# Performance work log

Measured on AMD Instinct MI355X. Metric: run time of the kernel, lower is better.

## Reference

```python
import jax, jax.numpy as jnp
import numpy as np

B, L, D, H = 4, 1024, 1024, 16
HD = D // H  # 64
MAX_LEN = 1024


def setup_inputs() -> dict:
    key = jax.random.key(0)
    k1, k2, k3, k4 = jax.random.split(key, 4)
    x = jax.random.normal(k1, (B, L, D), dtype=jnp.float32)
    W_qkv = jax.random.normal(k2, (D, 3 * D), dtype=jnp.float32) * (1.0 / np.sqrt(D))
    W_proj = jax.random.normal(k3, (D, D), dtype=jnp.float32) * (1.0 / np.sqrt(D))
    b_proj = jnp.zeros((D,), dtype=jnp.float32)
    rel_pos_emb = jax.random.normal(k4, (2 * MAX_LEN - 1, HD), dtype=jnp.float32)
    return {"x": x, "W_qkv": W_qkv, "W_proj": W_proj, "b_proj": b_proj,
            "rel_pos_emb": rel_pos_emb}


def reference(x, W_qkv, W_proj, b_proj, rel_pos_emb):
    b, l, d = x.shape
    scale = 1.0 / np.sqrt(HD)
    # fused qkv projection: [B, L, 3, H, HD]
    qkv = (x @ W_qkv).reshape(b, l, 3, H, HD)
    q = jnp.transpose(qkv[:, :, 0], (0, 2, 1, 3))  # [B, H, L, HD]
    k = jnp.transpose(qkv[:, :, 1], (0, 2, 1, 3))
    v = jnp.transpose(qkv[:, :, 2], (0, 2, 1, 3))
    # content scores
    attn = jnp.einsum('bhld,bhmd->bhlm', q, k) * scale
    # relative position scores: pos_indices[i, j] = (j - i) + (L - 1)
    pos_indices = (jnp.arange(l)[None, :] - jnp.arange(l)[:, None]) + (l - 1)
    rel_pos = rel_pos_emb[pos_indices]  # [L, L, HD]
    pos_attn = jnp.einsum('bhld,lkd->bhlk', q, rel_pos) * scale
    attn = jax.nn.softmax(attn + pos_attn, axis=-1)
    out = jnp.einsum('bhlm,bhmd->bhld', attn, v)  # [B, H, L, HD]
    out = jnp.transpose(out, (0, 2, 1, 3)).reshape(b, l, d)
    return out @ W_proj + b_proj
```

## Files before the change

kernel.cpp:

```cpp
#include <hip/hip_runtime.h>
#include <cstdint>

#define L_SEQ 1024
#define NH 16
#define HD 64
#define DMODEL 1024
#define BHS (L_SEQ * HD)

typedef __bf16 bf16x8 __attribute__((ext_vector_type(8)));
typedef float f32x4 __attribute__((ext_vector_type(4)));
typedef unsigned short u16x8 __attribute__((ext_vector_type(8)));

#define MFMA16(a, b, c) __builtin_amdgcn_mfma_f32_16x16x32_bf16((a), (b), (c), 0, 0, 0)

static __device__ __forceinline__ unsigned short f2b(float f) {
  unsigned int u = __builtin_bit_cast(unsigned int, f);
  u = (u + 0x7FFFu + ((u >> 16) & 1u)) >> 16;
  return (unsigned short)u;
}

static __device__ __forceinline__ bf16x8 ld8(const unsigned short* p) {
  return *(const bf16x8*)(p);
}

static __device__ __forceinline__ float bperm(int byteaddr, float v) {
  return __builtin_bit_cast(float,
      __builtin_amdgcn_ds_bpermute(byteaddr, __builtin_bit_cast(int, v)));
}

static __device__ __forceinline__ void gl_lds(const unsigned short* g,
                                              unsigned short* l) {
  auto gp = (const __attribute__((address_space(1))) unsigned int*)((uintptr_t)g);
  auto lp = (__attribute__((address_space(3))) unsigned int*)((uintptr_t)l);
  __builtin_amdgcn_global_load_lds(gp, lp, 16, 0, 0);
}

__global__ __launch_bounds__(256) void k_prep(
    const float* __restrict__ x,      unsigned short* __restrict__ xb,
    const float* __restrict__ relemb, unsigned short* __restrict__ eb,
    const float* __restrict__ Wqkv,   unsigned short* __restrict__ wtq,
    const float* __restrict__ Wproj,  unsigned short* __restrict__ wtp) {
  const int b = blockIdx.x, tid = threadIdx.x;
  if (b < 4224) {
    const float* src; unsigned short* dst; int i;
    if (b < 4096) { src = x; dst = xb; i = b * 256 + tid; }
    else          { src = relemb; dst = eb; i = (b - 4096) * 256 + tid; }
    const int n4 = (b < 4096) ? 1048576 : 32752;
    if (i < n4) {
      float4 v = *(const float4*)(src + (size_t)i * 4);
      ushort4 o;
      o.x = f2b(v.x); o.y = f2b(v.y); o.z = f2b(v.z); o.w = f2b(v.w);
      *(ushort4*)(dst + (size_t)i * 4) = o;
    }
  } else {
    __shared__ float tile[32][33];
    const float* src; unsigned short* dst; int bx, by, C;
    if (b < 7296) { src = Wqkv; dst = wtq; C = 3072; bx = (b - 4224) % 96; by = (b - 4224) / 96; }
    else          { src = Wproj; dst = wtp; C = 1024; bx = (b - 7296) % 32; by = (b - 7296) / 32; }
    const int R = 1024;
    const int c0 = bx * 32, r0 = by * 32;
    const int tx = tid & 31, ty = tid >> 5;
#pragma unroll
    for (int i = 0; i < 4; ++i)
      tile[ty + i * 8][tx] = src[(size_t)(r0 + ty + i * 8) * C + c0 + tx];
    __syncthreads();
#pragma unroll
    for (int i = 0; i < 4; ++i)
      dst[(size_t)(c0 + ty + i * 8) * R + r0 + tx] = f2b(tile[tx][ty + i * 8]);
  }
}

__global__ __launch_bounds__(256) void k_gemm_qkv(
    const unsigned short* __restrict__ xb,
    const unsigned short* __restrict__ wt,
    unsigned short* __restrict__ qw,
    unsigned short* __restrict__ kw,
    unsigned short* __restrict__ vtw) {
  __shared__ unsigned short As[128 * 64];
  __shared__ unsigned short Bs[128 * 64];
  const int tid = threadIdx.x;
  const int w = tid >> 6, lane = tid & 63;
  const int wm = w >> 1, wn = w & 1;
  const int lo = lane & 15, hi = lane >> 4;
  const int m0 = blockIdx.y * 128, n0 = blockIdx.x * 128;
  const int srow = lane >> 3, scol = lane & 7;

  f32x4 acc[4][4];
#pragma unroll
  for (int i = 0; i < 4; ++i)
#pragma unroll
    for (int j = 0; j < 4; ++j) acc[i][j] = (f32x4){0.f, 0.f, 0.f, 0.f};

  for (int kt = 0; kt < 16; ++kt) {
    const int k0 = kt * 64;
#pragma unroll
    for (int i = 0; i < 4; ++i) {
      const int slot = w * 4 + i;
      const int r = slot * 8 + srow;
      const int cs = (scol ^ (r & 7)) * 8;
      gl_lds(xb + (size_t)(m0 + r) * 1024 + k0 + cs, &As[slot * 512]);
      gl_lds(wt + (size_t)(n0 + r) * 1024 + k0 + cs, &Bs[slot * 512]);
    }
    __syncthreads();
    bf16x8 af[2][4], bg[2][4];
#pragma unroll
    for (int kk = 0; kk < 2; ++kk)
#pragma unroll
      for (int i = 0; i < 4; ++i) {
        const int ra = wm * 64 + i * 16 + lo;
        const int rb = wn * 64 + i * 16 + lo;
        af[kk][i] = ld8(&As[ra * 64 + (((kk * 4 + hi) ^ (lo & 7)) * 8)]);
        bg[kk][i] = ld8(&Bs[rb * 64 + (((kk * 4 + hi) ^ (lo & 7)) * 8)]);
      }
#pragma unroll
    for (int kk = 0; kk < 2; ++kk)
#pragma unroll
      for (int mf = 0; mf < 4; ++mf)
#pragma unroll
        for (int nf = 0; nf < 4; ++nf)
          acc[mf][nf] = MFMA16(af[kk][mf], bg[kk][nf], acc[mf][nf]);
    __syncthreads();
  }

  const int which = n0 >> 10;
#pragma unroll
  for (int mf = 0; mf < 4; ++mf) {
#pragma unroll
    for (int rr = 0; rr < 4; ++rr) {
      const int row = m0 + wm * 64 + mf * 16 + hi * 4 + rr;
      const int bb = row >> 10, ll = row & 1023;
#pragma unroll
      for (int nf = 0; nf < 4; ++nf) {
        const int col = n0 + wn * 64 + nf * 16 + lo;
        const int hc = col & 1023;
        const int hh = hc >> 6, dd = hc & 63;
        const unsigned short val = f2b(acc[mf][nf][rr]);
        const size_t bh = (size_t)(bb * NH + hh);
        if (which == 0)      qw[bh * BHS + ll * HD + dd] = val;
        else if (which == 1) kw[bh * BHS + ll * HD + dd] = val;
        else                 vtw[bh * BHS + dd * L_SEQ + ll] = val;
      }
    }
  }
}

__global__ __launch_bounds__(256, 2) void k_attn(
    const unsigned short* __restrict__ qw,
    const unsigned short* __restrict__ kw,
    const unsigned short* __restrict__ vtw,
    const unsigned short* __restrict__ ew,
    unsigned short* __restrict__ ow) {
  __shared__ unsigned short Kb[2][8192];
  __shared__ unsigned short Vb[2][8192];
  __shared__ unsigned short Ps[4][16][72];
  const int tid = threadIdx.x;
  const int w = tid >> 6, lane = tid & 63;
  const int lo = lane & 15, hi = lane >> 4;
  const int cw = lo & 7;
  const int lbid = (blockIdx.x & 7) * 64 + (blockIdx.x >> 3);
  const int bh = lbid >> 3, qb = lbid & 7;
  const int q0 = qb * 128;
  const int l0w = q0 + w * 32;
  const int bb = bh >> 4, hh = bh & 15;

  bf16x8 aQ[2][2];
#pragma unroll
  for (int s = 0; s < 2; ++s) {
    const unsigned short* qbase = qw + (size_t)bh * BHS + (l0w + s * 16 + lo) * HD;
    aQ[s][0] = ld8(qbase + hi * 8);
    aQ[s][1] = ld8(qbase + 32 + hi * 8);
  }

  const unsigned short* kbase = kw + (size_t)bh * BHS;
  const unsigned short* vbase = vtw + (size_t)bh * BHS;

  const u16x8 one_u = {0x3F80, 0x3F80, 0x3F80, 0x3F80,
                       0x3F80, 0x3F80, 0x3F80, 0x3F80};
  const bf16x8 onesf = __builtin_bit_cast(bf16x8, one_u);

  int gaddr[4];
  bool gpred[4];
#pragma unroll
  for (int r = 0; r < 4; ++r) {
    const int rho = hi * 4 + r;
    const int t = lo + 15 - rho;
    gaddr[r] = (hi * 16 + (t & 15)) * 4;
    gpred[r] = t >= 16;
  }

  auto stage = [&](int nxt, int it2) {
    const unsigned short* kt = kbase + (size_t)it2 * 128 * 64;
    const unsigned short* vt = vbase + it2 * 128;
#pragma unroll
    for (int i = 0; i < 4; ++i) {
      const int n = (w * 4 + i) * 64 + lane;
      const int r = n >> 3, c = n & 7;
      gl_lds(kt + r * 64 + ((c ^ (r & 7)) * 8), &Kb[nxt][(w * 4 + i) * 512]);
    }
#pragma unroll
    for (int i = 0; i < 4; ++i) {
      const int n = (w * 4 + i) * 64 + lane;
      const int m = n >> 3, c = n & 7;
      const int hhalf = m >> 6, dd = m & 63;
      gl_lds(vt + (size_t)dd * 1024 + hhalf * 64 + ((c ^ (m & 7)) * 8),
             &Vb[nxt][(w * 4 + i) * 512]);
    }
  };

  f32x4 acc_o[2][4];
  f32x4 acc_l[2];
#pragma unroll
  for (int s = 0; s < 2; ++s) {
    acc_l[s] = (f32x4){0.f, 0.f, 0.f, 0.f};
#pragma unroll
    for (int d = 0; d < 4; ++d) acc_o[s][d] = (f32x4){0.f, 0.f, 0.f, 0.f};
  }

  stage(0, 0);
  __syncthreads();

  auto pass = [&](int cur, int p, int tAbs) {
    const int xbase = tAbs * 64 - l0w + 992;
    bf16x8 ef[6][2];
#pragma unroll
    for (int f = 0; f < 6; ++f) {
      int er = xbase + f * 16 + lo;
      er = er > 2046 ? 2046 : er;
      const unsigned short* erow = ew + (size_t)er * HD + hi * 8;
      ef[f][0] = ld8(erow);
      ef[f][1] = ld8(erow + 32);
    }

    bf16x8 kf[4][2];
#pragma unroll
    for (int nf = 0; nf < 4; ++nf) {
      const unsigned short* kr = &Kb[cur][(p * 64 + nf * 16 + lo) * 64];
      kf[nf][0] = ld8(kr + ((hi ^ cw) * 8));
      kf[nf][1] = ld8(kr + (((4 + hi) ^ cw) * 8));
    }

    f32x4 acc_s[2][4];
    __builtin_amdgcn_s_setprio(1);
#pragma unroll
    for (int s = 0; s < 2; ++s)
#pragma unroll
      for (int nf = 0; nf < 4; ++nf) {
        f32x4 c = (f32x4){0.f, 0.f, 0.f, 0.f};
        c = MFMA16(aQ[s][0], kf[nf][0], c);
        c = MFMA16(aQ[s][1], kf[nf][1], c);
        acc_s[s][nf] = c;
      }
    __builtin_amdgcn_s_setprio(0);

    f32x4 G[2][5];
#pragma unroll
    for (int s = 0; s < 2; ++s) {
      const int fb = 1 - s;
#pragma unroll
      for (int gf = 0; gf < 5; ++gf) {
        f32x4 g = (f32x4){0.f, 0.f, 0.f, 0.f};
        g = MFMA16(aQ[s][0], ef[gf + fb][0], g);
        g = MFMA16(aQ[s][1], ef[gf + fb][1], g);
        G[s][gf] = g;
      }
    }
#pragma unroll
    for (int s = 0; s < 2; ++s)
#pragma unroll
      for (int gf = 0; gf < 5; ++gf)
#pragma unroll
        for (int r = 0; r < 4; ++r)
          G[s][gf][r] = bperm(gaddr[r], G[s][gf][r]);

    bf16x8 vf[4][2];
#pragma unroll
    for (int df = 0; df < 4; ++df) {
      const unsigned short* vr = &Vb[cur][(p * 64 + df * 16 + lo) * 64];
      vf[df][0] = ld8(vr + ((hi ^ cw) * 8));
      vf[df][1] = ld8(vr + (((4 + hi) ^ cw) * 8));
    }

#pragma unroll
    for (int s = 0; s < 2; ++s) {
#pragma unroll
      for (int nf = 0; nf < 4; ++nf)
#pragma unroll
        for (int r = 0; r < 4; ++r) {
          const float g = gpred[r] ? G[s][nf + 1][r] : G[s][nf][r];
          Ps[w][hi * 4 + r][nf * 16 + lo] =
              f2b(__expf((acc_s[s][nf][r] + g) * 0.125f));
        }
      const bf16x8 aP0 = ld8(&Ps[w][lo][hi * 8]);
      const bf16x8 aP1 = ld8(&Ps[w][lo][32 + hi * 8]);
      acc_l[s] = MFMA16(aP0, onesf, acc_l[s]);
      acc_l[s] = MFMA16(aP1, onesf, acc_l[s]);
      __builtin_amdgcn_s_setprio(1);
#pragma unroll
      for (int df = 0; df < 4; ++df) {
        acc_o[s][df] = MFMA16(aP0, vf[df][0], acc_o[s][df]);
        acc_o[s][df] = MFMA16(aP1, vf[df][1], acc_o[s][df]);
      }
      __builtin_amdgcn_s_setprio(0);
    }
  };

#pragma unroll 1
  for (int it = 0; it < 8; ++it) {
    const int cur = it & 1;
    pass(cur, 0, 2 * it);
    if (it < 7) stage(cur ^ 1, it + 1);
    pass(cur, 1, 2 * it + 1);
    __syncthreads();
  }

#pragma unroll
  for (int s = 0; s < 2; ++s)
#pragma unroll
    for (int r = 0; r < 4; ++r) {
      const int l = l0w + s * 16 + hi * 4 + r;
      const float inv = 1.f / acc_l[s][r];
      unsigned short* orow = ow + ((size_t)(bb * L_SEQ + l)) * DMODEL + hh * HD;
#pragma unroll
      for (int df = 0; df < 4; ++df)
        orow[df * 16 + lo] = f2b(acc_o[s][df][r] * inv);
    }
}

__global__ __launch_bounds__(256) void k_gemm_proj(
    const unsigned short* __restrict__ ob,
    const unsigned short* __restrict__ wt,
    const float* __restrict__ bias,
    float* __restrict__ out) {
  __shared__ unsigned short As[128 * 64];
  __shared__ unsigned short Bs[128 * 64];
  const int tid = threadIdx.x;
  const int w = tid >> 6, lane = tid & 63;
  const int wm = w >> 1, wn = w & 1;
  const int lo = lane & 15, hi = lane >> 4;
  const int m0 = blockIdx.y * 128, n0 = blockIdx.x * 128;
  const int srow = lane >> 3, scol = lane & 7;

  f32x4 acc[4][4];
#pragma unroll
  for (int i = 0; i < 4; ++i)
#pragma unroll
    for (int j = 0; j < 4; ++j) acc[i][j] = (f32x4){0.f, 0.f, 0.f, 0.f};

  for (int kt = 0; kt < 16; ++kt) {
    const int k0 = kt * 64;
#pragma unroll
    for (int i = 0; i < 4; ++i) {
      const int slot = w * 4 + i;
      const int r = slot * 8 + srow;
      const int cs = (scol ^ (r & 7)) * 8;
      gl_lds(ob + (size_t)(m0 + r) * 1024 + k0 + cs, &As[slot * 512]);
      gl_lds(wt + (size_t)(n0 + r) * 1024 + k0 + cs, &Bs[slot * 512]);
    }
    __syncthreads();
    bf16x8 af[2][4], bg[2][4];
#pragma unroll
    for (int kk = 0; kk < 2; ++kk)
#pragma unroll
      for (int i = 0; i < 4; ++i) {
        const int ra = wm * 64 + i * 16 + lo;
        const int rb = wn * 64 + i * 16 + lo;
        af[kk][i] = ld8(&As[ra * 64 + (((kk * 4 + hi) ^ (lo & 7)) * 8)]);
        bg[kk][i] = ld8(&Bs[rb * 64 + (((kk * 4 + hi) ^ (lo & 7)) * 8)]);
      }
#pragma unroll
    for (int kk = 0; kk < 2; ++kk)
#pragma unroll
      for (int mf = 0; mf < 4; ++mf)
#pragma unroll
        for (int nf = 0; nf < 4; ++nf)
          acc[mf][nf] = MFMA16(af[kk][mf], bg[kk][nf], acc[mf][nf]);
    __syncthreads();
  }

#pragma unroll
  for (int mf = 0; mf < 4; ++mf) {
#pragma unroll
    for (int rr = 0; rr < 4; ++rr) {
      const int row = m0 + wm * 64 + mf * 16 + hi * 4 + rr;
#pragma unroll
      for (int nf = 0; nf < 4; ++nf) {
        const int col = n0 + wn * 64 + nf * 16 + lo;
        out[(size_t)row * 1024 + col] = acc[mf][nf][rr] + bias[col];
      }
    }
  }
}

extern "C" void kernel_launch(void* const* d_in, const int* in_sizes, int n_in,
                              void* d_out, int out_size, void* d_ws, size_t ws_size,
                              hipStream_t stream) {
  const float* x      = (const float*)d_in[0];
  const float* Wqkv   = (const float*)d_in[1];
  const float* Wproj  = (const float*)d_in[2];
  const float* bproj  = (const float*)d_in[3];
  const float* relemb = (const float*)d_in[4];
  float* out = (float*)d_out;

  char* ws = (char*)d_ws;
  size_t off = 0;
  auto alloc = [&](size_t bytes) -> unsigned short* {
    unsigned short* p = (unsigned short*)(ws + off);
    off += (bytes + 255) & ~(size_t)255;
    return p;
  };
  unsigned short* xb  = alloc((size_t)4096 * 1024 * 2);
  unsigned short* wtq = alloc((size_t)3072 * 1024 * 2);
  unsigned short* wtp = alloc((size_t)1024 * 1024 * 2);
  unsigned short* eb  = alloc((size_t)2047 * 64 * 2);
  unsigned short* qw_ = alloc((size_t)64 * BHS * 2);
  unsigned short* kw_ = alloc((size_t)64 * BHS * 2);
  unsigned short* vtw = alloc((size_t)64 * BHS * 2);
  unsigned short* ow  = alloc((size_t)4096 * 1024 * 2);

  k_prep<<<8320, 256, 0, stream>>>(x, xb, relemb, eb, Wqkv, wtq, Wproj, wtp);
  k_gemm_qkv<<<dim3(24, 32), 256, 0, stream>>>(xb, wtq, qw_, kw_, vtw);
  k_attn<<<512, 256, 0, stream>>>(qw_, kw_, vtw, eb, ow);
  k_gemm_proj<<<dim3(8, 32), 256, 0, stream>>>(ow, wtp, bproj, out);
}
```

Measured before the change: 124.6 us.

## Load V fragments directly from global and transpose P via ds_read_b64_tr_b16

Removes the V staging through LDS: each wave now reads its V^T fragments straight from global memory at the start of every pass, which halves the shared-memory footprint and the async copy traffic. The P tile write is changed to packed 4-element stores in a transposed layout, read back with the LDS transpose-read instruction in inline asm instead of scattered scalar stores followed by row reads. The aim is fewer LDS bank conflicts and instructions, and possibly higher occupancy. The cost is that V reads now go to global/L2 memory without double-buffer prefetch, and the inline asm waits on all LDS operations.

```diff
diff --git a/kernel.cpp b/kernel.cpp
--- a/kernel.cpp
+++ b/kernel.cpp
@@ -10,6 +10,7 @@
 typedef __bf16 bf16x8 __attribute__((ext_vector_type(8)));
 typedef float f32x4 __attribute__((ext_vector_type(4)));
 typedef unsigned short u16x8 __attribute__((ext_vector_type(8)));
+typedef unsigned int uint32x2 __attribute__((ext_vector_type(2)));
 
 #define MFMA16(a, b, c) __builtin_amdgcn_mfma_f32_16x16x32_bf16((a), (b), (c), 0, 0, 0)
 
@@ -151,8 +152,7 @@
     const unsigned short* __restrict__ ew,
     unsigned short* __restrict__ ow) {
   __shared__ unsigned short Kb[2][8192];
-  __shared__ unsigned short Vb[2][8192];
-  __shared__ unsigned short Ps[4][16][72];
+  __shared__ unsigned short Pt[4][1024];
   const int tid = threadIdx.x;
   const int w = tid >> 6, lane = tid & 63;
   const int lo = lane & 15, hi = lane >> 4;
@@ -178,6 +178,9 @@
                        0x3F80, 0x3F80, 0x3F80, 0x3F80};
   const bf16x8 onesf = __builtin_bit_cast(bf16x8, one_u);
 
+  auto ptb = (__attribute__((address_space(3))) const unsigned short*)
+                 ((uintptr_t)&Pt[w][0]) + hi * 128 + lo * 4;
+
   int gaddr[4];
   bool gpred[4];
 #pragma unroll
@@ -190,21 +193,12 @@
 
   auto stage = [&](int nxt, int it2) {
     const unsigned short* kt = kbase + (size_t)it2 * 128 * 64;
-    const unsigned short* vt = vbase + it2 * 128;
 #pragma unroll
     for (int i = 0; i < 4; ++i) {
       const int n = (w * 4 + i) * 64 + lane;
       const int r = n >> 3, c = n & 7;
       gl_lds(kt + r * 64 + ((c ^ (r & 7)) * 8), &Kb[nxt][(w * 4 + i) * 512]);
     }
-#pragma unroll
-    for (int i = 0; i < 4; ++i) {
-      const int n = (w * 4 + i) * 64 + lane;
-      const int m = n >> 3, c = n & 7;
-      const int hhalf = m >> 6, dd = m & 63;
-      gl_lds(vt + (size_t)dd * 1024 + hhalf * 64 + ((c ^ (m & 7)) * 8),
-             &Vb[nxt][(w * 4 + i) * 512]);
-    }
   };
 
   f32x4 acc_o[2][4];
@@ -220,7 +214,17 @@
   __syncthreads();
 
   auto pass = [&](int cur, int p, int tAbs) {
-    const int xbase = tAbs * 64 - l0w + 992;
+    const int j0 = tAbs * 64;
+
+    bf16x8 vf[4][2];
+#pragma unroll
+    for (int df = 0; df < 4; ++df) {
+      const unsigned short* vr = vbase + (size_t)(df * 16 + lo) * L_SEQ + j0 + hi * 8;
+      vf[df][0] = ld8(vr);
+      vf[df][1] = ld8(vr + 32);
+    }
+
+    const int xbase = j0 - l0w + 992;
     bf16x8 ef[6][2];
 #pragma unroll
     for (int f = 0; f < 6; ++f) {
@@ -272,26 +276,41 @@
         for (int r = 0; r < 4; ++r)
           G[s][gf][r] = bperm(gaddr[r], G[s][gf][r]);
 
-    bf16x8 vf[4][2];
-#pragma unroll
-    for (int df = 0; df < 4; ++df) {
-      const unsigned short* vr = &Vb[cur][(p * 64 + df * 16 + lo) * 64];
-      vf[df][0] = ld8(vr + ((hi ^ cw) * 8));
-      vf[df][1] = ld8(vr + (((4 + hi) ^ cw) * 8));
-    }
-
 #pragma unroll
     for (int s = 0; s < 2; ++s) {
 #pragma unroll
-      for (int nf = 0; nf < 4; ++nf)
-#pragma unroll
-        for (int r = 0; r < 4; ++r) {
-          const float g = gpred[r] ? G[s][nf + 1][r] : G[s][nf][r];
-          Ps[w][hi * 4 + r][nf * 16 + lo] =
-              f2b(__expf((acc_s[s][nf][r] + g) * 0.125f));
+      for (int nf = 0; nf < 4; ++nf) {
+        ushort4 pk;
+        {
+          const float g0 = gpred[0] ? G[s][nf + 1][0] : G[s][nf][0];
+          const float g1 = gpred[1] ? G[s][nf + 1][1] : G[s][nf][1];
+          const float g2 = gpred[2] ? G[s][nf + 1][2] : G[s][nf][2];
+          const float g3 = gpred[3] ? G[s][nf + 1][3] : G[s][nf][3];
+          pk.x = f2b(__expf((acc_s[s][nf][0] + g0) * 0.125f));
+          pk.y = f2b(__expf((acc_s[s][nf][1] + g1) * 0.125f));
+          pk.z = f2b(__expf((acc_s[s][nf][2] + g2) * 0.125f));
+          pk.w = f2b(__expf((acc_s[s][nf][3] + g3) * 0.125f));
         }
-      const bf16x8 aP0 = ld8(&Ps[w][lo][hi * 8]);
-      const bf16x8 aP1 = ld8(&Ps[w][lo][32 + hi * 8]);
+        *(ushort4*)(&Pt[w][(16 * nf + lo) * 16 + 4 * hi]) = pk;
+      }
+
+      uint32x2 t0, t1, t2, t3;
+      asm volatile(
+          "ds_read_b64_tr_b16 %0, %4\n\t"
+          "ds_read_b64_tr_b16 %1, %4 offset:128\n\t"
+          "ds_read_b64_tr_b16 %2, %4 offset:1024\n\t"
+          "ds_read_b64_tr_b16 %3, %4 offset:1152\n\t"
+          "s_waitcnt lgkmcnt(0)"
+          : "=v"(t0), "=v"(t1), "=v"(t2), "=v"(t3)
+          : "v"(ptb)
+          : "memory");
+      __builtin_amdgcn_sched_barrier(0);
+      uint4 q0, q1;
+      q0.x = t0.x; q0.y = t0.y; q0.z = t1.x; q0.w = t1.y;
+      q1.x = t2.x; q1.y = t2.y; q1.z = t3.x; q1.w = t3.y;
+      const bf16x8 aP0 = __builtin_bit_cast(bf16x8, q0);
+      const bf16x8 aP1 = __builtin_bit_cast(bf16x8, q1);
+
       acc_l[s] = MFMA16(aP0, onesf, acc_l[s]);
       acc_l[s] = MFMA16(aP1, onesf, acc_l[s]);
       __builtin_amdgcn_s_setprio(1);
```

After: 151.7 us. 1.22x slower.
